# Kernel tuning notes

Hardware: AMD Instinct MI355X
Metric: run time of the kernel (lower is better)

Reference implementation:

```python
import jax, jax.numpy as jnp
import numpy as np

N_MELS = 80
FORMANT_START, FORMANT_END = 10, 50
W_L1, W_DELTA, W_DELTA2, W_SC, W_BAND, FORMANT_W = 1.0, 0.5, 0.25, 0.5, 1.0, 2.0
EPS = 1e-8


def _masked_mean(x, mask):
    # mask broadcasts to x's shape; count = sum of the broadcast mask
    n = jnp.maximum(jnp.sum(jnp.broadcast_to(mask, x.shape)), 1.0)
    return jnp.sum(x * mask) / n


def setup_inputs() -> dict:
    key = jax.random.key(0)
    k1, k2, k3 = jax.random.split(key, 3)
    B, T, D = 64, 4000, N_MELS
    pred_mel = jax.random.normal(k1, (B, T, D), dtype=jnp.float32)
    target_mel = jax.random.normal(k2, (B, T, D), dtype=jnp.float32)
    lengths = jax.random.randint(k3, (B,), T // 2, T + 1)
    mel_mask = (jnp.arange(T)[None, :] < lengths[:, None]).astype(jnp.float32)
    band_weights = jnp.ones((D,), dtype=jnp.float32).at[FORMANT_START:FORMANT_END].set(FORMANT_W)
    return {"pred_mel": pred_mel, "target_mel": target_mel, "mel_mask": mel_mask,
            "band_weights": band_weights}


def reference(pred_mel, target_mel, mel_mask, band_weights):
    mask3 = mel_mask[:, :, None]                      # (B,T,1)

    l1 = jnp.abs(pred_mel - target_mel)               # (B,T,D)
    l1_loss = _masked_mean(l1, mask3)

    # 1st-order deltas
    dp = pred_mel[:, 1:] - pred_mel[:, :-1]
    dt = target_mel[:, 1:] - target_mel[:, :-1]
    dmask = (mel_mask[:, 1:] * mel_mask[:, :-1])[:, :, None]
    delta_loss = _masked_mean(jnp.abs(dp - dt), dmask)

    # 2nd-order deltas
    d2p = dp[:, 1:] - dp[:, :-1]
    d2t = dt[:, 1:] - dt[:, :-1]
    d2mask = (mel_mask[:, 2:] * mel_mask[:, 1:-1] * mel_mask[:, :-2])[:, :, None]
    delta2_loss = _masked_mean(jnp.abs(d2p - d2t), d2mask)

    # spectral convergence
    diff = (pred_mel - target_mel) * mask3
    tgt_m = target_mel * mask3
    n = jnp.maximum(jnp.sum(jnp.broadcast_to(mask3, pred_mel.shape)), 1.0)
    sc_num = jnp.sqrt(jnp.sum(diff * diff) / n)
    sc_den = jnp.maximum(jnp.sqrt(jnp.sum(tgt_m * tgt_m) / n), EPS)
    sc_loss = sc_num / sc_den

    # band-weighted L1
    w = band_weights[None, None, :]
    band_loss = _masked_mean(l1 * w, mask3) / jnp.mean(band_weights)

    # energy (per-frame mean over mel bins)
    e_l1 = jnp.abs(pred_mel.mean(axis=-1) - target_mel.mean(axis=-1))  # (B,T)
    energy_loss = _masked_mean(e_l1, mel_mask)

    return (W_L1 * l1_loss + W_DELTA * delta_loss + W_DELTA2 * delta2_loss
            + W_SC * sc_loss + W_BAND * band_loss + 0.5 * energy_loss)
```

## Files before the change

### kernel.cpp

```cpp
#include <hip/hip_runtime.h>
#include <math.h>

#define D_MELS 80
#define F4ROW  20
#define T_DIM  4000
#define NQM    7
#define NTHR   256
#define RPI    14

template<int CTRL>
__device__ __forceinline__ float dppf(float v) {
    return __int_as_float(__builtin_amdgcn_update_dpp(
        0, __float_as_int(v), CTRL, 0xF, 0xF, true));
}
#define ROW_SHL1 0x101
#define ROW_SHL2 0x102
#define ROW_SHL4 0x104
#define ROW_SHL8 0x108
#define ROW_SHR1 0x111
#define ROW_SHR2 0x112

__device__ __forceinline__ float wave_sum(float v) {
    v += dppf<ROW_SHL8>(v);
    v += dppf<ROW_SHL4>(v);
    v += dppf<ROW_SHL2>(v);
    v += dppf<ROW_SHL1>(v);
    v += __shfl_xor(v, 16, 64);
    v += __shfl_xor(v, 32, 64);
    return v;
}

__global__ __launch_bounds__(NTHR) void mel_flags(
    const float* __restrict__ mask, int* __restrict__ bflag,
    float* __restrict__ cpart, int BT, int nmb, int rowsPerMB, int nfb)
{
    const int tid  = threadIdx.x;
    const int lane = tid & 63;
    const int wv   = tid >> 6;
    const int g    = blockIdx.x * (NTHR / 64) + wv;

    float cm = 0.f, cdm = 0.f, cd2m = 0.f;
    int   fl = 0;

    if (g < nmb) {
        const int rlo = g * rowsPerMB;
        int rhi = rlo + rowsPerMB; if (rhi > BT) rhi = BT;
        for (int r = rlo - 2 + lane; r < rhi; r += 64) {
            if (r < 0) continue;
            float m = mask[r];
            fl |= (m != 0.f);
            if (r >= rlo && m != 0.f) {
                int t = r % T_DIM;
                cm += m;
                if (t >= 1) {
                    float m1 = mask[r - 1];
                    cdm += m * m1;
                    if (t >= 2) cd2m += m * m1 * mask[r - 2];
                }
            }
        }
    }

    const bool anyl = __any(fl != 0);
    #pragma unroll
    for (int off = 32; off > 0; off >>= 1) {
        cm   += __shfl_down(cm,   off, 64);
        cdm  += __shfl_down(cdm,  off, 64);
        cd2m += __shfl_down(cd2m, off, 64);
    }
    if (g < nmb && lane == 0) bflag[g] = anyl ? 1 : 0;

    __shared__ float cred[NTHR / 64][3];
    if (lane == 0) { cred[wv][0] = cm; cred[wv][1] = cdm; cred[wv][2] = cd2m; }
    __syncthreads();
    if (tid < 3) {
        float s = 0.f;
        #pragma unroll
        for (int w2 = 0; w2 < NTHR / 64; ++w2) s += cred[w2][tid];
        cpart[tid * nfb + blockIdx.x] = s;
    }
}

__global__ __launch_bounds__(NTHR, 4) void mel_loss_main(
    const float* __restrict__ pred, const float* __restrict__ tgt,
    const float* __restrict__ mask, const int* __restrict__ bflag,
    float* __restrict__ partial, int BT, int Jtot, int K, int nmb)
{
    const int tid = threadIdx.x;

    if (!bflag[blockIdx.x]) {
        if (tid < NQM) partial[tid * nmb + blockIdx.x] = 0.f;
        return;
    }

    const int lane = tid & 63;
    const int qtr  = lane >> 4;
    const int rw   = lane & 15;
    const int wv   = tid >> 6;
    const int gw   = blockIdx.x * (NTHR / 64) + wv;

    const float4* p4 = (const float4*)pred;
    const float4* q4 = (const float4*)tgt;

    float v_l1 = 0.f, v_frr = 0.f, v_diff2 = 0.f, v_tgt2 = 0.f, v_energy = 0.f;
    float v_d = 0.f, v_d2 = 0.f;

    const int j0 = gw * K;
    for (int s = 0; s < K; ++s) {
        const int j = j0 + s;
        if (j >= Jtot) break;
        const int r = j * RPI - 2 + rw;
        const int rload = r < 0 ? 0 : (r >= BT ? BT - 1 : r);

        const size_t rowb = (size_t)rload * F4ROW + qtr;
        float  mload = mask[rload];
        float4 P[5], Q[5];
        #pragma unroll
        for (int k = 0; k < 5; ++k) P[k] = p4[rowb + 4 * k];
        #pragma unroll
        for (int k = 0; k < 5; ++k) Q[k] = q4[rowb + 4 * k];

        if (!__any(mload != 0.0f)) continue;

        const int t = rload % T_DIM;
        const float m1 = dppf<ROW_SHR1>(mload);
        const float m2 = dppf<ROW_SHR2>(mload);
        const bool contrib = (rw >= 2) && (r < BT);
        const float mt   = contrib ? mload : 0.f;
        const float dmv  = (t >= 1) ? mt * m1 : 0.f;
        const float d2mv = (t >= 2) ? dmv * m2 : 0.f;

        float l1r = 0.f, frr = 0.f, sqr = 0.f, t2r = 0.f, er = 0.f, dr = 0.f, d2r = 0.f;
        #pragma unroll
        for (int k = 0; k < 5; ++k) {
            float e0 = P[k].x - Q[k].x, e1 = P[k].y - Q[k].y,
                  e2 = P[k].z - Q[k].z, e3 = P[k].w - Q[k].w;

            float f0 = dppf<ROW_SHR1>(e0), f1 = dppf<ROW_SHR1>(e1),
                  f2 = dppf<ROW_SHR1>(e2), f3 = dppf<ROW_SHR1>(e3);
            float g0 = dppf<ROW_SHR2>(e0), g1 = dppf<ROW_SHR2>(e1),
                  g2 = dppf<ROW_SHR2>(e2), g3 = dppf<ROW_SHR2>(e3);

            float a0 = fabsf(e0), a1 = fabsf(e1), a2 = fabsf(e2), a3 = fabsf(e3);
            l1r += a0 + a1 + a2 + a3;
            const int d0 = (k << 4) + (qtr << 2);
            frr += ((unsigned)(d0 + 0 - 10) < 40u ? a0 : 0.f)
                 + ((unsigned)(d0 + 1 - 10) < 40u ? a1 : 0.f)
                 + ((unsigned)(d0 + 2 - 10) < 40u ? a2 : 0.f)
                 + ((unsigned)(d0 + 3 - 10) < 40u ? a3 : 0.f);
            sqr += e0 * e0 + e1 * e1 + e2 * e2 + e3 * e3;
            t2r += Q[k].x * Q[k].x + Q[k].y * Q[k].y + Q[k].z * Q[k].z + Q[k].w * Q[k].w;
            er  += e0 + e1 + e2 + e3;
            dr  += fabsf(e0 - f0) + fabsf(e1 - f1) + fabsf(e2 - f2) + fabsf(e3 - f3);
            d2r += fabsf(e0 - 2.f * f0 + g0) + fabsf(e1 - 2.f * f1 + g1)
                 + fabsf(e2 - 2.f * f2 + g2) + fabsf(e3 - 2.f * f3 + g3);
        }

        v_l1    += l1r * mt;
        v_frr   += frr * mt;
        v_diff2 += sqr * mt;
        v_tgt2  += t2r * mt;
        v_d     += dr * dmv;
        v_d2    += d2r * d2mv;

        er += __shfl_xor(er, 16, 64);
        er += __shfl_xor(er, 32, 64);
        if (qtr == 0) v_energy += fabsf(er) * mt;
    }

    float vals[NQM] = {v_l1, v_frr, v_diff2, v_tgt2, v_energy, v_d, v_d2};
    #pragma unroll
    for (int q = 0; q < NQM; ++q) vals[q] = wave_sum(vals[q]);

    __shared__ float red[NTHR / 64][NQM];
    if (lane == 0) {
        #pragma unroll
        for (int q = 0; q < NQM; ++q) red[wv][q] = vals[q];
    }
    __syncthreads();
    if (tid < NQM) {
        float s = 0.f;
        #pragma unroll
        for (int w2 = 0; w2 < NTHR / 64; ++w2) s += red[w2][tid];
        partial[tid * nmb + blockIdx.x] = s;
    }
}

__global__ __launch_bounds__(640) void mel_loss_finalize(
    const float* __restrict__ partial, const float* __restrict__ cpart,
    const float* __restrict__ w, float* __restrict__ out, int nmb, int nfb)
{
    const int tid = threadIdx.x;
    const int wv  = tid >> 6;
    const int lane = tid & 63;
    __shared__ float fin[10];

    float s = 0.f;
    if (wv < NQM) {
        for (int i = lane; i < nmb; i += 64) s += partial[wv * nmb + i];
    } else {
        for (int i = lane; i < nfb; i += 64) s += cpart[(wv - NQM) * nfb + i];
    }
    #pragma unroll
    for (int off = 32; off > 0; off >>= 1) s += __shfl_down(s, off, 64);
    if (lane == 0 && wv < 10) fin[wv] = s;
    __syncthreads();

    if (tid == 0) {
        float l1s = fin[0], frrs = fin[1], diff2 = fin[2], tgt2 = fin[3];
        float energys = fin[4], ds = fin[5], d2s = fin[6];
        float ms = fin[7], dms = fin[8], d2ms = fin[9];

        float wsum = 0.f;
        for (int d = 0; d < D_MELS; ++d) wsum += w[d];
        float wmean = wsum / (float)D_MELS;

        float n1  = fmaxf(ms   * (float)D_MELS, 1.f);
        float nd  = fmaxf(dms  * (float)D_MELS, 1.f);
        float nd2 = fmaxf(d2ms * (float)D_MELS, 1.f);

        float l1_loss     = l1s / n1;
        float delta_loss  = ds / nd;
        float delta2_loss = d2s / nd2;
        float sc_num = sqrtf(diff2 / n1);
        float sc_den = fmaxf(sqrtf(tgt2 / n1), 1e-8f);
        float sc_loss = sc_num / sc_den;
        float band_loss = ((l1s + frrs) / n1) / wmean;
        float energy_loss = (energys / (float)D_MELS) / fmaxf(ms, 1.f);

        out[0] = 1.0f * l1_loss + 0.5f * delta_loss + 0.25f * delta2_loss
               + 0.5f * sc_loss + 1.0f * band_loss + 0.5f * energy_loss;
    }
}

extern "C" void kernel_launch(void* const* d_in, const int* in_sizes, int n_in,
                              void* d_out, int out_size, void* d_ws, size_t ws_size,
                              hipStream_t stream) {
    const float* pred = (const float*)d_in[0];
    const float* tgt  = (const float*)d_in[1];
    const float* mask = (const float*)d_in[2];
    const float* w    = (const float*)d_in[3];
    int BT = in_sizes[2];

    int Jtot = (BT + RPI - 1) / RPI;

    int K, nmb, nfb;
    size_t need;
    for (K = 2;; K *= 2) {
        int nwaves = (Jtot + K - 1) / K;
        nmb = (nwaves + (NTHR / 64) - 1) / (NTHR / 64);
        nfb = (nmb + (NTHR / 64) - 1) / (NTHR / 64);
        need = (size_t)(NQM * nmb + 3 * nfb) * sizeof(float) + (size_t)nmb * sizeof(int);
        if (need <= ws_size || K >= Jtot) break;
    }
    const int rowsPerMB = (NTHR / 64) * K * RPI;

    float* partial = (float*)d_ws;
    float* cpart   = partial + NQM * nmb;
    int*   bflag   = (int*)(cpart + 3 * nfb);

    mel_flags<<<nfb, NTHR, 0, stream>>>(mask, bflag, cpart, BT, nmb, rowsPerMB, nfb);
    mel_loss_main<<<nmb, NTHR, 0, stream>>>(pred, tgt, mask, bflag, partial, BT, Jtot, K, nmb);
    mel_loss_finalize<<<1, 640, 0, stream>>>(partial, cpart, w, (float*)d_out, nmb, nfb);
}
```

Before: 193.1 us.

## Restructure main loss kernel to flat coalesced 16-row groups with neighbor reloads

Replaces the 14-useful-of-16-row overlapping tile with DPP row shifts by a flat layout where each wave processes 16-row groups as contiguous float4 chunks. The previous and second-previous rows are fetched with extra global loads instead of cross-lane DPP, and next-chunk loads are double-buffered in registers. Per-frame energy sums go through LDS atomics, and launch bounds drop to 2 blocks per SM. The extra neighbor loads triple load instructions (mostly cache hits) and add LDS atomics, in exchange for fully coalesced accesses and no wasted halo rows. It also drops the skip of chunks whose mask is all zero, so masked-out frames are now loaded and computed.

```diff
diff --git a/kernel.cpp b/kernel.cpp
--- a/kernel.cpp
+++ b/kernel.cpp
@@ -6,7 +6,7 @@
 #define T_DIM  4000
 #define NQM    7
 #define NTHR   256
-#define RPI    14
+#define GPW    4
 
 template<int CTRL>
 __device__ __forceinline__ float dppf(float v) {
@@ -17,8 +17,6 @@
 #define ROW_SHL2 0x102
 #define ROW_SHL4 0x104
 #define ROW_SHL8 0x108
-#define ROW_SHR1 0x111
-#define ROW_SHR2 0x112
 
 __device__ __forceinline__ float wave_sum(float v) {
     v += dppf<ROW_SHL8>(v);
@@ -81,10 +79,10 @@
     }
 }
 
-__global__ __launch_bounds__(NTHR, 4) void mel_loss_main(
+__global__ __launch_bounds__(NTHR, 2) void mel_loss_main(
     const float* __restrict__ pred, const float* __restrict__ tgt,
     const float* __restrict__ mask, const int* __restrict__ bflag,
-    float* __restrict__ partial, int BT, int Jtot, int K, int nmb)
+    float* __restrict__ partial, int BT, int ngroups, int nmb)
 {
     const int tid = threadIdx.x;
 
@@ -94,78 +92,102 @@
     }
 
     const int lane = tid & 63;
-    const int qtr  = lane >> 4;
-    const int rw   = lane & 15;
     const int wv   = tid >> 6;
-    const int gw   = blockIdx.x * (NTHR / 64) + wv;
 
     const float4* p4 = (const float4*)pred;
     const float4* q4 = (const float4*)tgt;
+    const long ntot4 = (long)BT * F4ROW;
+
+    int  row_off[5];
+    float4 bsel[5];
+    #pragma unroll
+    for (int k = 0; k < 5; ++k) {
+        int j = lane + 64 * k;
+        row_off[k] = j / 20;
+        int d0 = (j % 20) * 4;
+        bsel[k].x = ((unsigned)(d0 + 0 - 10) < 40u) ? 1.f : 0.f;
+        bsel[k].y = ((unsigned)(d0 + 1 - 10) < 40u) ? 1.f : 0.f;
+        bsel[k].z = ((unsigned)(d0 + 2 - 10) < 40u) ? 1.f : 0.f;
+        bsel[k].w = ((unsigned)(d0 + 3 - 10) < 40u) ? 1.f : 0.f;
+    }
+
+    __shared__ float rs[NTHR / 64][16];
 
     float v_l1 = 0.f, v_frr = 0.f, v_diff2 = 0.f, v_tgt2 = 0.f, v_energy = 0.f;
     float v_d = 0.f, v_d2 = 0.f;
 
-    const int j0 = gw * K;
-    for (int s = 0; s < K; ++s) {
-        const int j = j0 + s;
-        if (j >= Jtot) break;
-        const int r = j * RPI - 2 + rw;
-        const int rload = r < 0 ? 0 : (r >= BT ? BT - 1 : r);
-
-        const size_t rowb = (size_t)rload * F4ROW + qtr;
-        float  mload = mask[rload];
-        float4 P[5], Q[5];
-        #pragma unroll
-        for (int k = 0; k < 5; ++k) P[k] = p4[rowb + 4 * k];
-        #pragma unroll
-        for (int k = 0; k < 5; ++k) Q[k] = q4[rowb + 4 * k];
-
-        if (!__any(mload != 0.0f)) continue;
-
-        const int t = rload % T_DIM;
-        const float m1 = dppf<ROW_SHR1>(mload);
-        const float m2 = dppf<ROW_SHR2>(mload);
-        const bool contrib = (rw >= 2) && (r < BT);
-        const float mt   = contrib ? mload : 0.f;
-        const float dmv  = (t >= 1) ? mt * m1 : 0.f;
-        const float d2mv = (t >= 2) ? dmv * m2 : 0.f;
-
-        float l1r = 0.f, frr = 0.f, sqr = 0.f, t2r = 0.f, er = 0.f, dr = 0.f, d2r = 0.f;
+    const int gbase = (blockIdx.x * (NTHR / 64) + wv) * GPW;
+
+    for (int gi = 0; gi < GPW; ++gi) {
+        const int g = gbase + gi;
+        if (g >= ngroups) break;
+        const int  rg = g * 16;
+        const int  tg = rg % T_DIM;
+        const long fb = (long)g * 320;
+
+        if (lane < 16) rs[wv][lane] = 0.f;
+
+        float4 P[2][3], Q[2][3];
+        float  M[2][3];
+
+        #define LOADK(kk, b)                                                      \
+        {                                                                         \
+            long i0 = fb + lane + 64 * (kk);                                      \
+            if (i0 >= ntot4) i0 = ntot4 - 1;                                      \
+            long i1 = i0 - 20; if (i1 < 0) i1 = 0;                                \
+            long i2 = i0 - 40; if (i2 < 0) i2 = 0;                                \
+            P[b][0] = p4[i0]; Q[b][0] = q4[i0];                                   \
+            P[b][1] = p4[i1]; Q[b][1] = q4[i1];                                   \
+            P[b][2] = p4[i2]; Q[b][2] = q4[i2];                                   \
+            int r = rg + row_off[kk]; int rc = r < BT ? r : BT - 1;               \
+            int r1 = rc - 1; if (r1 < 0) r1 = 0;                                  \
+            int r2 = rc - 2; if (r2 < 0) r2 = 0;                                  \
+            M[b][0] = mask[rc]; M[b][1] = mask[r1]; M[b][2] = mask[r2];           \
+        }
+
+        LOADK(0, 0)
         #pragma unroll
         for (int k = 0; k < 5; ++k) {
-            float e0 = P[k].x - Q[k].x, e1 = P[k].y - Q[k].y,
-                  e2 = P[k].z - Q[k].z, e3 = P[k].w - Q[k].w;
-
-            float f0 = dppf<ROW_SHR1>(e0), f1 = dppf<ROW_SHR1>(e1),
-                  f2 = dppf<ROW_SHR1>(e2), f3 = dppf<ROW_SHR1>(e3);
-            float g0 = dppf<ROW_SHR2>(e0), g1 = dppf<ROW_SHR2>(e1),
-                  g2 = dppf<ROW_SHR2>(e2), g3 = dppf<ROW_SHR2>(e3);
+            if (k < 4) {
+                if ((k & 1) == 0) LOADK(k + 1, 1)
+                else              LOADK(k + 1, 0)
+            }
+            const int b = k & 1;
+            const int r = rg + row_off[k];
+            int t = tg + row_off[k]; if (t >= T_DIM) t -= T_DIM;
+
+            float e0 = P[b][0].x - Q[b][0].x, e1 = P[b][0].y - Q[b][0].y,
+                  e2 = P[b][0].z - Q[b][0].z, e3 = P[b][0].w - Q[b][0].w;
+            float f0 = P[b][1].x - Q[b][1].x, f1 = P[b][1].y - Q[b][1].y,
+                  f2 = P[b][1].z - Q[b][1].z, f3 = P[b][1].w - Q[b][1].w;
+            float g0 = P[b][2].x - Q[b][2].x, g1 = P[b][2].y - Q[b][2].y,
+                  g2 = P[b][2].z - Q[b][2].z, g3 = P[b][2].w - Q[b][2].w;
+
+            const float mt   = (r < BT) ? M[b][0] : 0.f;
+            const float dmv  = (t >= 1) ? mt * M[b][1] : 0.f;
+            const float d2mv = (t >= 2) ? dmv * M[b][2] : 0.f;
 
             float a0 = fabsf(e0), a1 = fabsf(e1), a2 = fabsf(e2), a3 = fabsf(e3);
-            l1r += a0 + a1 + a2 + a3;
-            const int d0 = (k << 4) + (qtr << 2);
-            frr += ((unsigned)(d0 + 0 - 10) < 40u ? a0 : 0.f)
-                 + ((unsigned)(d0 + 1 - 10) < 40u ? a1 : 0.f)
-                 + ((unsigned)(d0 + 2 - 10) < 40u ? a2 : 0.f)
-                 + ((unsigned)(d0 + 3 - 10) < 40u ? a3 : 0.f);
-            sqr += e0 * e0 + e1 * e1 + e2 * e2 + e3 * e3;
-            t2r += Q[k].x * Q[k].x + Q[k].y * Q[k].y + Q[k].z * Q[k].z + Q[k].w * Q[k].w;
-            er  += e0 + e1 + e2 + e3;
-            dr  += fabsf(e0 - f0) + fabsf(e1 - f1) + fabsf(e2 - f2) + fabsf(e3 - f3);
-            d2r += fabsf(e0 - 2.f * f0 + g0) + fabsf(e1 - 2.f * f1 + g1)
-                 + fabsf(e2 - 2.f * f2 + g2) + fabsf(e3 - 2.f * f3 + g3);
-        }
-
-        v_l1    += l1r * mt;
-        v_frr   += frr * mt;
-        v_diff2 += sqr * mt;
-        v_tgt2  += t2r * mt;
-        v_d     += dr * dmv;
-        v_d2    += d2r * d2mv;
-
-        er += __shfl_xor(er, 16, 64);
-        er += __shfl_xor(er, 32, 64);
-        if (qtr == 0) v_energy += fabsf(er) * mt;
+            v_l1    += (a0 + a1 + a2 + a3) * mt;
+            v_frr   += (a0 * bsel[k].x + a1 * bsel[k].y
+                      + a2 * bsel[k].z + a3 * bsel[k].w) * mt;
+            v_diff2 += (e0 * e0 + e1 * e1 + e2 * e2 + e3 * e3) * mt;
+            v_tgt2  += (Q[b][0].x * Q[b][0].x + Q[b][0].y * Q[b][0].y
+                      + Q[b][0].z * Q[b][0].z + Q[b][0].w * Q[b][0].w) * mt;
+            v_d     += (fabsf(e0 - f0) + fabsf(e1 - f1)
+                      + fabsf(e2 - f2) + fabsf(e3 - f3)) * dmv;
+            v_d2    += (fabsf(e0 - 2.f * f0 + g0) + fabsf(e1 - 2.f * f1 + g1)
+                      + fabsf(e2 - 2.f * f2 + g2) + fabsf(e3 - 2.f * f3 + g3)) * d2mv;
+
+            atomicAdd(&rs[wv][row_off[k]], e0 + e1 + e2 + e3);
+        }
+        #undef LOADK
+
+        if (lane < 16) {
+            int r = rg + lane;
+            float mm = (r < BT) ? mask[r] : 0.f;
+            v_energy += fabsf(rs[wv][lane]) * mm;
+        }
     }
 
     float vals[NQM] = {v_l1, v_frr, v_diff2, v_tgt2, v_energy, v_d, v_d2};
@@ -242,24 +264,17 @@
     const float* w    = (const float*)d_in[3];
     int BT = in_sizes[2];
 
-    int Jtot = (BT + RPI - 1) / RPI;
-
-    int K, nmb, nfb;
-    size_t need;
-    for (K = 2;; K *= 2) {
-        int nwaves = (Jtot + K - 1) / K;
-        nmb = (nwaves + (NTHR / 64) - 1) / (NTHR / 64);
-        nfb = (nmb + (NTHR / 64) - 1) / (NTHR / 64);
-        need = (size_t)(NQM * nmb + 3 * nfb) * sizeof(float) + (size_t)nmb * sizeof(int);
-        if (need <= ws_size || K >= Jtot) break;
-    }
-    const int rowsPerMB = (NTHR / 64) * K * RPI;
+    int ngroups = (BT + 15) / 16;
+    int wavesN  = (ngroups + GPW - 1) / GPW;
+    int nmb     = (wavesN + (NTHR / 64) - 1) / (NTHR / 64);
+    int nfb     = (nmb + (NTHR / 64) - 1) / (NTHR / 64);
+    int rowsPerMB = (NTHR / 64) * GPW * 16;
 
     float* partial = (float*)d_ws;
     float* cpart   = partial + NQM * nmb;
     int*   bflag   = (int*)(cpart + 3 * nfb);
 
     mel_flags<<<nfb, NTHR, 0, stream>>>(mask, bflag, cpart, BT, nmb, rowsPerMB, nfb);
-    mel_loss_main<<<nmb, NTHR, 0, stream>>>(pred, tgt, mask, bflag, partial, BT, Jtot, K, nmb);
+    mel_loss_main<<<nmb, NTHR, 0, stream>>>(pred, tgt, mask, bflag, partial, BT, ngroups, nmb);
     mel_loss_finalize<<<1, 640, 0, stream>>>(partial, cpart, w, (float*)d_out, nmb, nfb);
 }
```

Result: slower. 202.8 us (+5.0%).
